# Kernel tuning notes

Measured on AMD Instinct MI355X. Metric: run time of the kernel, lower is better.

## Reference

```python
import jax, jax.numpy as jnp
import numpy as np

B, N = 32768, 512

def setup_inputs() -> dict:
    key = jax.random.key(0)
    k1, k2, k3, k4 = jax.random.split(key, 4)
    log_sigma_hat = jax.random.normal(k1, (B, N), dtype=jnp.float32)
    sigma = jax.random.normal(k2, (B, N), dtype=jnp.float32)
    SR = jax.random.normal(k3, (N,), dtype=jnp.float32)
    # well-conditioned invertible Gamma (covariance-like): A A^T / N + I
    A = jax.random.normal(k4, (N, N), dtype=jnp.float32)
    Gamma = A @ A.T / N + jnp.eye(N, dtype=jnp.float32)
    return {"log_sigma_hat": log_sigma_hat, "sigma": sigma, "SR": SR, "Gamma": Gamma, "k": 12}

def reference(log_sigma_hat, sigma, SR, Gamma, k):
    # r[t] = exp(sigma[t]) / exp(log_sigma_hat[t])  -> [B, N]
    r = jnp.exp(sigma - log_sigma_hat)
    Gamma_inv = jnp.linalg.inv(Gamma)
    v = Gamma_inv @ SR           # [N]  Gamma^{-1} SR
    u = Gamma_inv.T @ SR         # [N]  (SR^T Gamma^{-1})^T
    # first  = SR^T Gamma^{-1} diag(r) SR / k = sum(u * r * SR)
    first = (r * (u * SR)).sum(axis=-1) / k
    # second = SR^T Gamma^{-1} diag(r) Gamma diag(r) Gamma^{-1} SR / (2k)
    w = r * v                                     # [B, N] = diag(r) v
    Gw = jnp.einsum('ij,bj->bi', Gamma, w)        # [B, N] = Gamma diag(r) v
    second = (u * (r * Gw)).sum(axis=-1) / (2 * k)
    utils = first - second                        # [B]
    return -utils.mean()
```

## Files before the change

kernel.cpp:

```cpp
#include <hip/hip_runtime.h>
#include <hip/hip_bf16.h>
#include <stdint.h>

#define BB 32768
#define NN 512
#define CHEB_IT 10

typedef __attribute__((ext_vector_type(8))) short bf16x8;
typedef __attribute__((ext_vector_type(4))) float f32x4;

__device__ __forceinline__ void gld_lds16(const void* g, void* l) {
  typedef __attribute__((address_space(1))) const unsigned int gas_u32;
  typedef __attribute__((address_space(3))) unsigned int las_u32;
  __builtin_amdgcn_global_load_lds((gas_u32*)(uintptr_t)g,
                                   (las_u32*)(uint32_t)(uintptr_t)l, 16, 0, 0);
}

__device__ __forceinline__ unsigned short f2bf(float x) {
  __hip_bfloat16 h = __float2bfloat16(x);
  return *reinterpret_cast<unsigned short*>(&h);
}

__device__ __forceinline__ float bf2f(unsigned short u) {
  return __uint_as_float(((unsigned)u) << 16);
}

__device__ __forceinline__ float wave_reduce(float v) {
#pragma unroll
  for (int off = 32; off > 0; off >>= 1) v += __shfl_xor(v, off, 64);
  return v;
}

__device__ void cheb_phase(const unsigned short* __restrict__ Gbf,
                           const float* __restrict__ SR, float* __restrict__ v_out,
                           float* __restrict__ appart, unsigned int* __restrict__ ctr,
                           float* sm) {
  float* sp = sm;
  float* apw = sm + 512;
  const int t = threadIdx.x;
  const int m = blockIdx.x;
  const int rg = t >> 7;
  const int c0 = (t & 127) * 4;
  const int row0 = m * 128;
  const float theta = 3.16f, delta = 2.19f;
  const float sigma1 = theta / delta;
  float rho = delta / theta;
  float r = SR[t];
  float x = 0.f;
  float p = r * (1.0f / theta);
  for (int k = 0; k < CHEB_IT; ++k) {
    sp[t] = p;
    __syncthreads();
    float a0 = 0, a1 = 0, a2 = 0, a3 = 0;
    for (int j = 0; j < 128; j += 32) {
#pragma unroll
      for (int jj = 0; jj < 8; ++jj) {
        const int lr = j + jj * 4 + rg;
        ushort4 u = *(const ushort4*)(Gbf + (size_t)(row0 + lr) * NN + c0);
        float pv = sp[row0 + lr];
        a0 += bf2f(u.x) * pv; a1 += bf2f(u.y) * pv;
        a2 += bf2f(u.z) * pv; a3 += bf2f(u.w) * pv;
      }
    }
    *(float4*)(apw + rg * 512 + c0) = make_float4(a0, a1, a2, a3);
    __syncthreads();
    float apm = apw[t] + apw[512 + t] + apw[1024 + t] + apw[1536 + t];
    float* buf = appart + (k & 1) * 2048 + m * 512;
    __hip_atomic_store(buf + t, apm, __ATOMIC_RELAXED, __HIP_MEMORY_SCOPE_AGENT);
    __threadfence();
    __syncthreads();
    if (t == 0)
      __hip_atomic_fetch_add(ctr, 1u, __ATOMIC_RELEASE, __HIP_MEMORY_SCOPE_AGENT);
    if (t == 0) {
      const unsigned tgt = 4u * (unsigned)(k + 1);
      int guard = 0;
      while (__hip_atomic_load(ctr, __ATOMIC_ACQUIRE, __HIP_MEMORY_SCOPE_AGENT) < tgt) {
        if (++guard > (1 << 27)) break;
        __builtin_amdgcn_s_sleep(8);
      }
    }
    __syncthreads();
    const float* rbuf = appart + (k & 1) * 2048;
    float w = __hip_atomic_load(rbuf + t, __ATOMIC_RELAXED, __HIP_MEMORY_SCOPE_AGENT) +
              __hip_atomic_load(rbuf + 512 + t, __ATOMIC_RELAXED, __HIP_MEMORY_SCOPE_AGENT) +
              __hip_atomic_load(rbuf + 1024 + t, __ATOMIC_RELAXED, __HIP_MEMORY_SCOPE_AGENT) +
              __hip_atomic_load(rbuf + 1536 + t, __ATOMIC_RELAXED, __HIP_MEMORY_SCOPE_AGENT);
    x += p;
    r -= w;
    const float rho_new = 1.f / (2.f * sigma1 - rho);
    p = rho_new * rho * p + (2.f * rho_new / delta) * r;
    rho = rho_new;
    __syncthreads();
  }
  if (m == 0) v_out[t] = x;
}

__global__ __launch_bounds__(256) void k0_prep(
    const float* __restrict__ Gam, unsigned short* __restrict__ Gbf,
    float* __restrict__ small_zero) {
  const int t = threadIdx.x, b = blockIdx.x;
  const size_t base = ((size_t)b * 256 + t) * 8;
  float4 g0 = *(const float4*)(Gam + base);
  float4 g1 = *(const float4*)(Gam + base + 4);
  *(ushort4*)(Gbf + base) = make_ushort4(f2bf(g0.x), f2bf(g0.y), f2bf(g0.z), f2bf(g0.w));
  *(ushort4*)(Gbf + base + 4) = make_ushort4(f2bf(g1.x), f2bf(g1.y), f2bf(g1.z), f2bf(g1.w));
  if (b == 0)
    for (int i = t; i < 8960; i += 256) small_zero[i] = 0.f;
}

__global__ __launch_bounds__(512) void k1_rexp(
    const float* __restrict__ lsh, const float* __restrict__ sig,
    const float* __restrict__ SR, const unsigned short* __restrict__ Gbf,
    unsigned short* __restrict__ Rb, float* __restrict__ v_out,
    float* __restrict__ colsum, float* __restrict__ appart,
    unsigned int* __restrict__ ctr) {
  __shared__ __align__(16) float sm[2560];
  if (blockIdx.x < 4) {
    cheb_phase(Gbf, SR, v_out, appart, ctr, sm);
    return;
  }
  const int t = threadIdx.x;
  const int wb = blockIdx.x - 4;
  const size_t base = (size_t)wb * 16384;
  float c0 = 0.f, c1 = 0.f, c2 = 0.f, c3 = 0.f;
#pragma unroll
  for (int j = 0; j < 8; ++j) {
    const size_t idx = base + (size_t)j * 2048 + (size_t)t * 4;
    float4 sv = *(const float4*)(sig + idx);
    float4 lv = *(const float4*)(lsh + idx);
    float r0 = __expf(sv.x - lv.x), r1 = __expf(sv.y - lv.y);
    float r2 = __expf(sv.z - lv.z), r3 = __expf(sv.w - lv.w);
    *(ushort4*)(Rb + idx) = make_ushort4(f2bf(r0), f2bf(r1), f2bf(r2), f2bf(r3));
    c0 += r0; c1 += r1; c2 += r2; c3 += r3;
  }
  float* part = sm;
  *(float4*)(part + (t >> 7) * 512 + (t & 127) * 4) = make_float4(c0, c1, c2, c3);
  __syncthreads();
  float s = part[t] + part[512 + t] + part[1024 + t] + part[1536 + t];
  atomicAdd(&colsum[(wb & 7) * NN + t], s);
}

__global__ __launch_bounds__(256) void k1b_gprep(
    const float* __restrict__ Gam, const float* __restrict__ v,
    unsigned short* __restrict__ Gp) {
  const int t = threadIdx.x;
  const size_t e = ((size_t)blockIdx.x * 256 + t) * 8;
  const int i = (int)(e >> 9), j = (int)(e & 511);
  const float vi = v[i];
  float4 va = *(const float4*)(v + j);
  float4 vb = *(const float4*)(v + j + 4);
  float4 g0 = *(const float4*)(Gam + e);
  float4 g1 = *(const float4*)(Gam + e + 4);
  *(ushort4*)(Gp + e) = make_ushort4(f2bf(g0.x * vi * va.x), f2bf(g0.y * vi * va.y),
                                     f2bf(g0.z * vi * va.z), f2bf(g0.w * vi * va.w));
  *(ushort4*)(Gp + e + 4) = make_ushort4(f2bf(g1.x * vi * vb.x), f2bf(g1.y * vi * vb.y),
                                         f2bf(g1.z * vi * vb.z), f2bf(g1.w * vi * vb.w));
}

__global__ __launch_bounds__(512) void k2_gemm(
    const unsigned short* __restrict__ Rb, const unsigned short* __restrict__ Gp,
    float* __restrict__ secsum) {
  __shared__ __align__(16) unsigned short smem[32768];
  const int bid = blockIdx.x;
  const int nt_ = (bid >> 3) & 3;
  const int bs_ = (bid & 7) + ((bid >> 5) << 3);
  const int b0 = bs_ * 128;
  const int n0 = nt_ * 128;
  const int t = threadIdx.x, lane = t & 63, wv = t >> 6;
  const int wi = (wv & 3) * 32, wj = (wv >> 2) * 64;
  const int lm = lane & 15, lq = lane >> 4;
  const int xr = lm & 7;
  const int srow = t >> 3, sc = t & 7;
  const int scol = (sc ^ (srow & 7)) * 8;
  f32x4 acc[2][4];
#pragma unroll
  for (int a = 0; a < 2; ++a)
#pragma unroll
    for (int b = 0; b < 4; ++b) acc[a][b] = (f32x4){0.f, 0.f, 0.f, 0.f};

#define STAGE(kk, buf)                                                                   \
  {                                                                                      \
    unsigned short* As_ = smem + (buf)*16384;                                            \
    unsigned short* Bs_ = As_ + 8192;                                                    \
    gld_lds16(Rb + (size_t)(b0 + srow) * NN + (kk) + scol, As_ + srow * 64 + sc * 8);    \
    gld_lds16(Rb + (size_t)(b0 + 64 + srow) * NN + (kk) + scol,                          \
              As_ + (64 + srow) * 64 + sc * 8);                                          \
    gld_lds16(Gp + (size_t)(n0 + srow) * NN + (kk) + scol, Bs_ + srow * 64 + sc * 8);    \
    gld_lds16(Gp + (size_t)(n0 + 64 + srow) * NN + (kk) + scol,                          \
              Bs_ + (64 + srow) * 64 + sc * 8);                                          \
  }

  STAGE(0, 0);
  __syncthreads();
  for (int c = 0; c < 8; ++c) {
    if (c < 7) STAGE((c + 1) * 64, (c + 1) & 1);
    const unsigned short* As = smem + (c & 1) * 16384;
    const unsigned short* Bs = As + 8192;
#pragma unroll
    for (int s = 0; s < 2; ++s) {
      bf16x8 af[2], bfr[4];
#pragma unroll
      for (int g = 0; g < 2; ++g)
        af[g] = *(const bf16x8*)(As + (wi + g * 16 + lm) * 64 + ((s * 4 + lq) ^ xr) * 8);
#pragma unroll
      for (int g = 0; g < 4; ++g)
        bfr[g] = *(const bf16x8*)(Bs + (wj + g * 16 + lm) * 64 + ((s * 4 + lq) ^ xr) * 8);
#pragma unroll
      for (int gm = 0; gm < 2; ++gm)
#pragma unroll
        for (int gn = 0; gn < 4; ++gn)
          acc[gm][gn] = __builtin_amdgcn_mfma_f32_16x16x32_bf16(af[gm], bfr[gn], acc[gm][gn], 0, 0, 0);
    }
    __syncthreads();
  }
#undef STAGE

  float s_ = 0.f;
#pragma unroll
  for (int gm = 0; gm < 2; ++gm) {
    const int rb = b0 + wi + gm * 16 + lq * 4;
#pragma unroll
    for (int gn = 0; gn < 4; ++gn) {
      const int cl = n0 + wj + gn * 16 + lm;
      const unsigned short* rp = Rb + (size_t)rb * NN + cl;
      s_ += acc[gm][gn][0] * bf2f(rp[0]);
      s_ += acc[gm][gn][1] * bf2f(rp[NN]);
      s_ += acc[gm][gn][2] * bf2f(rp[2 * NN]);
      s_ += acc[gm][gn][3] * bf2f(rp[3 * NN]);
    }
  }
  s_ = wave_reduce(s_);
  float* red = (float*)smem;
  if (lane == 0) red[wv] = s_;
  __syncthreads();
  if (t == 0) {
    float a = 0;
#pragma unroll
    for (int i = 0; i < 8; ++i) a += red[i];
    atomicAdd(&secsum[bid & 63], a);
  }
}

__global__ __launch_bounds__(512) void k4_final(
    const float* __restrict__ colsum, const float* __restrict__ v,
    const float* __restrict__ SR, const float* __restrict__ secsum,
    const int* __restrict__ kp, float* __restrict__ out) {
  __shared__ float red[8];
  const int t = threadIdx.x;
  float cs = 0;
#pragma unroll
  for (int bk = 0; bk < 8; ++bk) cs += colsum[bk * NN + t];
  float f = (cs * (1.0f / BB)) * v[t] * SR[t];
  f = wave_reduce(f);
  if ((t & 63) == 0) red[t >> 6] = f;
  float h = 0.f;
  if (t < 64) {
    h = secsum[t];
    h = wave_reduce(h);
  }
  __syncthreads();
  if (t == 0) {
    float first = 0;
#pragma unroll
    for (int i = 0; i < 8; ++i) first += red[i];
    float kk = (float)kp[0];
    float sec = h / ((float)BB * 2.0f * kk);
    out[0] = -(first / kk - sec);
  }
}

extern "C" void kernel_launch(void* const* d_in, const int* in_sizes, int n_in,
                              void* d_out, int out_size, void* d_ws, size_t ws_size,
                              hipStream_t stream) {
  const float* lsh = (const float*)d_in[0];
  const float* sig = (const float*)d_in[1];
  const float* SR = (const float*)d_in[2];
  const float* Gam = (const float*)d_in[3];
  const int* kp = (const int*)d_in[4];
  char* ws = (char*)d_ws;
  float* colsum = (float*)ws;
  float* secsum = colsum + 4096;
  float* v = secsum + 64;
  unsigned int* ctr = (unsigned int*)(v + 512);
  float* appart = (float*)(ctr + 16);
  unsigned short* Gbf = (unsigned short*)(ws + (64 << 10));
  unsigned short* Gp = (unsigned short*)(ws + (64 << 10) + (512 << 10));
  unsigned short* Rb = (unsigned short*)(ws + (64 << 10) + (1024 << 10));

  k0_prep<<<128, 256, 0, stream>>>(Gam, Gbf, colsum);
  k1_rexp<<<1028, 512, 0, stream>>>(lsh, sig, SR, Gbf, Rb, v, colsum, appart, ctr);
  k1b_gprep<<<128, 256, 0, stream>>>(Gam, v, Gp);
  k2_gemm<<<1024, 512, 0, stream>>>(Rb, Gp, secsum);
  k4_final<<<1, 512, 0, stream>>>(colsum, v, SR, secsum, kp, (float*)d_out);
}
```

Before: 224.7 us.

## Single-block Chebyshev solve, 1024-thread rexp blocks, 256x128 GEMM tiles

The Chebyshev solve moves from four blocks synchronised through global atomics and spin-waits to one 1024-thread block that does the whole matvec with an LDS reduction, removing the inter-block barrier traffic. The exp kernel uses 1024-thread blocks and half as many of them. The GEMM tile grows from 128x128 to 256x128, giving more reuse of the Gp tile and fewer blocks, but it drops the double-buffered global-to-LDS prefetch in favour of a single buffer with load-then-sync. The 16 accumulators per wave raise register pressure, and the loss of load/compute overlap could offset the reuse gain.

```diff
diff --git a/kernel.cpp b/kernel.cpp
--- a/kernel.cpp
+++ b/kernel.cpp
@@ -33,66 +33,49 @@
 
 __device__ void cheb_phase(const unsigned short* __restrict__ Gbf,
                            const float* __restrict__ SR, float* __restrict__ v_out,
-                           float* __restrict__ appart, unsigned int* __restrict__ ctr,
                            float* sm) {
   float* sp = sm;
   float* apw = sm + 512;
   const int t = threadIdx.x;
-  const int m = blockIdx.x;
   const int rg = t >> 7;
   const int c0 = (t & 127) * 4;
-  const int row0 = m * 128;
   const float theta = 3.16f, delta = 2.19f;
   const float sigma1 = theta / delta;
   float rho = delta / theta;
-  float r = SR[t];
-  float x = 0.f;
-  float p = r * (1.0f / theta);
+  float x = 0.f, r = 0.f, p = 0.f;
+  if (t < 512) {
+    r = SR[t];
+    p = r * (1.0f / theta);
+  }
   for (int k = 0; k < CHEB_IT; ++k) {
-    sp[t] = p;
+    if (t < 512) sp[t] = p;
     __syncthreads();
     float a0 = 0, a1 = 0, a2 = 0, a3 = 0;
-    for (int j = 0; j < 128; j += 32) {
+    for (int j = 0; j < NN; j += 64) {
 #pragma unroll
       for (int jj = 0; jj < 8; ++jj) {
-        const int lr = j + jj * 4 + rg;
-        ushort4 u = *(const ushort4*)(Gbf + (size_t)(row0 + lr) * NN + c0);
-        float pv = sp[row0 + lr];
+        const int row = j + jj * 8 + rg;
+        ushort4 u = *(const ushort4*)(Gbf + (size_t)row * NN + c0);
+        float pv = sp[row];
         a0 += bf2f(u.x) * pv; a1 += bf2f(u.y) * pv;
         a2 += bf2f(u.z) * pv; a3 += bf2f(u.w) * pv;
       }
     }
     *(float4*)(apw + rg * 512 + c0) = make_float4(a0, a1, a2, a3);
     __syncthreads();
-    float apm = apw[t] + apw[512 + t] + apw[1024 + t] + apw[1536 + t];
-    float* buf = appart + (k & 1) * 2048 + m * 512;
-    __hip_atomic_store(buf + t, apm, __ATOMIC_RELAXED, __HIP_MEMORY_SCOPE_AGENT);
-    __threadfence();
-    __syncthreads();
-    if (t == 0)
-      __hip_atomic_fetch_add(ctr, 1u, __ATOMIC_RELEASE, __HIP_MEMORY_SCOPE_AGENT);
-    if (t == 0) {
-      const unsigned tgt = 4u * (unsigned)(k + 1);
-      int guard = 0;
-      while (__hip_atomic_load(ctr, __ATOMIC_ACQUIRE, __HIP_MEMORY_SCOPE_AGENT) < tgt) {
-        if (++guard > (1 << 27)) break;
-        __builtin_amdgcn_s_sleep(8);
-      }
-    }
-    __syncthreads();
-    const float* rbuf = appart + (k & 1) * 2048;
-    float w = __hip_atomic_load(rbuf + t, __ATOMIC_RELAXED, __HIP_MEMORY_SCOPE_AGENT) +
-              __hip_atomic_load(rbuf + 512 + t, __ATOMIC_RELAXED, __HIP_MEMORY_SCOPE_AGENT) +
-              __hip_atomic_load(rbuf + 1024 + t, __ATOMIC_RELAXED, __HIP_MEMORY_SCOPE_AGENT) +
-              __hip_atomic_load(rbuf + 1536 + t, __ATOMIC_RELAXED, __HIP_MEMORY_SCOPE_AGENT);
-    x += p;
-    r -= w;
-    const float rho_new = 1.f / (2.f * sigma1 - rho);
-    p = rho_new * rho * p + (2.f * rho_new / delta) * r;
-    rho = rho_new;
-    __syncthreads();
-  }
-  if (m == 0) v_out[t] = x;
+    if (t < 512) {
+      float ap = 0.f;
+#pragma unroll
+      for (int g = 0; g < 8; ++g) ap += apw[g * 512 + t];
+      x += p;
+      r -= ap;
+      const float rho_new = 1.f / (2.f * sigma1 - rho);
+      p = rho_new * rho * p + (2.f * rho_new / delta) * r;
+      rho = rho_new;
+    }
+    __syncthreads();
+  }
+  if (t < 512) v_out[t] = x;
 }
 
 __global__ __launch_bounds__(256) void k0_prep(
@@ -105,27 +88,28 @@
   *(ushort4*)(Gbf + base) = make_ushort4(f2bf(g0.x), f2bf(g0.y), f2bf(g0.z), f2bf(g0.w));
   *(ushort4*)(Gbf + base + 4) = make_ushort4(f2bf(g1.x), f2bf(g1.y), f2bf(g1.z), f2bf(g1.w));
   if (b == 0)
-    for (int i = t; i < 8960; i += 256) small_zero[i] = 0.f;
-}
-
-__global__ __launch_bounds__(512) void k1_rexp(
+    for (int i = t; i < 4672; i += 256) small_zero[i] = 0.f;
+}
+
+__global__ __launch_bounds__(1024) void k1_rexp(
     const float* __restrict__ lsh, const float* __restrict__ sig,
     const float* __restrict__ SR, const unsigned short* __restrict__ Gbf,
     unsigned short* __restrict__ Rb, float* __restrict__ v_out,
-    float* __restrict__ colsum, float* __restrict__ appart,
-    unsigned int* __restrict__ ctr) {
-  __shared__ __align__(16) float sm[2560];
-  if (blockIdx.x < 4) {
-    cheb_phase(Gbf, SR, v_out, appart, ctr, sm);
+    float* __restrict__ colsum) {
+  __shared__ __align__(16) float sm[4608];
+  if (blockIdx.x == 0) {
+    cheb_phase(Gbf, SR, v_out, sm);
     return;
   }
   const int t = threadIdx.x;
-  const int wb = blockIdx.x - 4;
-  const size_t base = (size_t)wb * 16384;
+  const int wb = blockIdx.x - 1;
+  const int g = t >> 7;
+  const int c = (t & 127) * 4;
+  const size_t base = (size_t)wb * 32768;
   float c0 = 0.f, c1 = 0.f, c2 = 0.f, c3 = 0.f;
 #pragma unroll
   for (int j = 0; j < 8; ++j) {
-    const size_t idx = base + (size_t)j * 2048 + (size_t)t * 4;
+    const size_t idx = base + (size_t)(g + 8 * j) * 512 + c;
     float4 sv = *(const float4*)(sig + idx);
     float4 lv = *(const float4*)(lsh + idx);
     float r0 = __expf(sv.x - lv.x), r1 = __expf(sv.y - lv.y);
@@ -134,10 +118,14 @@
     c0 += r0; c1 += r1; c2 += r2; c3 += r3;
   }
   float* part = sm;
-  *(float4*)(part + (t >> 7) * 512 + (t & 127) * 4) = make_float4(c0, c1, c2, c3);
-  __syncthreads();
-  float s = part[t] + part[512 + t] + part[1024 + t] + part[1536 + t];
-  atomicAdd(&colsum[(wb & 7) * NN + t], s);
+  *(float4*)(part + g * 512 + c) = make_float4(c0, c1, c2, c3);
+  __syncthreads();
+  if (t < 512) {
+    float s = 0.f;
+#pragma unroll
+    for (int gg = 0; gg < 8; ++gg) s += part[gg * 512 + t];
+    atomicAdd(&colsum[(wb & 7) * NN + t], s);
+  }
 }
 
 __global__ __launch_bounds__(256) void k1b_gprep(
@@ -160,64 +148,60 @@
 __global__ __launch_bounds__(512) void k2_gemm(
     const unsigned short* __restrict__ Rb, const unsigned short* __restrict__ Gp,
     float* __restrict__ secsum) {
-  __shared__ __align__(16) unsigned short smem[32768];
+  __shared__ __align__(16) unsigned short smem[24576];
   const int bid = blockIdx.x;
   const int nt_ = (bid >> 3) & 3;
   const int bs_ = (bid & 7) + ((bid >> 5) << 3);
-  const int b0 = bs_ * 128;
+  const int b0 = bs_ * 256;
   const int n0 = nt_ * 128;
   const int t = threadIdx.x, lane = t & 63, wv = t >> 6;
-  const int wi = (wv & 3) * 32, wj = (wv >> 2) * 64;
+  const int wi = (wv >> 1) * 64;
+  const int wj = (wv & 1) * 64;
   const int lm = lane & 15, lq = lane >> 4;
   const int xr = lm & 7;
   const int srow = t >> 3, sc = t & 7;
   const int scol = (sc ^ (srow & 7)) * 8;
-  f32x4 acc[2][4];
-#pragma unroll
-  for (int a = 0; a < 2; ++a)
+  unsigned short* As = smem;
+  unsigned short* Bs = smem + 16384;
+  f32x4 acc[4][4];
+#pragma unroll
+  for (int a = 0; a < 4; ++a)
 #pragma unroll
     for (int b = 0; b < 4; ++b) acc[a][b] = (f32x4){0.f, 0.f, 0.f, 0.f};
 
-#define STAGE(kk, buf)                                                                   \
-  {                                                                                      \
-    unsigned short* As_ = smem + (buf)*16384;                                            \
-    unsigned short* Bs_ = As_ + 8192;                                                    \
-    gld_lds16(Rb + (size_t)(b0 + srow) * NN + (kk) + scol, As_ + srow * 64 + sc * 8);    \
-    gld_lds16(Rb + (size_t)(b0 + 64 + srow) * NN + (kk) + scol,                          \
-              As_ + (64 + srow) * 64 + sc * 8);                                          \
-    gld_lds16(Gp + (size_t)(n0 + srow) * NN + (kk) + scol, Bs_ + srow * 64 + sc * 8);    \
-    gld_lds16(Gp + (size_t)(n0 + 64 + srow) * NN + (kk) + scol,                          \
-              Bs_ + (64 + srow) * 64 + sc * 8);                                          \
-  }
-
-  STAGE(0, 0);
-  __syncthreads();
-  for (int c = 0; c < 8; ++c) {
-    if (c < 7) STAGE((c + 1) * 64, (c + 1) & 1);
-    const unsigned short* As = smem + (c & 1) * 16384;
-    const unsigned short* Bs = As + 8192;
+  for (int ch = 0; ch < 8; ++ch) {
+    const int kk = ch * 64;
+    if (ch) __syncthreads();
+#pragma unroll
+    for (int ps = 0; ps < 4; ++ps)
+      gld_lds16(Rb + (size_t)(b0 + ps * 64 + srow) * NN + kk + scol,
+                As + (ps * 64 + srow) * 64 + sc * 8);
+#pragma unroll
+    for (int ps = 0; ps < 2; ++ps)
+      gld_lds16(Gp + (size_t)(n0 + ps * 64 + srow) * NN + kk + scol,
+                Bs + (ps * 64 + srow) * 64 + sc * 8);
+    __syncthreads();
 #pragma unroll
     for (int s = 0; s < 2; ++s) {
-      bf16x8 af[2], bfr[4];
-#pragma unroll
-      for (int g = 0; g < 2; ++g)
+      bf16x8 af[4], bfr[4];
+#pragma unroll
+      for (int g = 0; g < 4; ++g)
         af[g] = *(const bf16x8*)(As + (wi + g * 16 + lm) * 64 + ((s * 4 + lq) ^ xr) * 8);
 #pragma unroll
       for (int g = 0; g < 4; ++g)
         bfr[g] = *(const bf16x8*)(Bs + (wj + g * 16 + lm) * 64 + ((s * 4 + lq) ^ xr) * 8);
 #pragma unroll
-      for (int gm = 0; gm < 2; ++gm)
+      for (int gm = 0; gm < 4; ++gm)
 #pragma unroll
         for (int gn = 0; gn < 4; ++gn)
           acc[gm][gn] = __builtin_amdgcn_mfma_f32_16x16x32_bf16(af[gm], bfr[gn], acc[gm][gn], 0, 0, 0);
     }
-    __syncthreads();
-  }
-#undef STAGE
+  }
+  __syncthreads();
 
   float s_ = 0.f;
 #pragma unroll
-  for (int gm = 0; gm < 2; ++gm) {
+  for (int gm = 0; gm < 4; ++gm) {
     const int rb = b0 + wi + gm * 16 + lq * 4;
 #pragma unroll
     for (int gn = 0; gn < 4; ++gn) {
@@ -281,15 +265,13 @@
   float* colsum = (float*)ws;
   float* secsum = colsum + 4096;
   float* v = secsum + 64;
-  unsigned int* ctr = (unsigned int*)(v + 512);
-  float* appart = (float*)(ctr + 16);
-  unsigned short* Gbf = (unsigned short*)(ws + (64 << 10));
-  unsigned short* Gp = (unsigned short*)(ws + (64 << 10) + (512 << 10));
-  unsigned short* Rb = (unsigned short*)(ws + (64 << 10) + (1024 << 10));
+  unsigned short* Gbf = (unsigned short*)(ws + (32 << 10));
+  unsigned short* Gp = (unsigned short*)(ws + (32 << 10) + (512 << 10));
+  unsigned short* Rb = (unsigned short*)(ws + (32 << 10) + (1024 << 10));
 
   k0_prep<<<128, 256, 0, stream>>>(Gam, Gbf, colsum);
-  k1_rexp<<<1028, 512, 0, stream>>>(lsh, sig, SR, Gbf, Rb, v, colsum, appart, ctr);
+  k1_rexp<<<513, 1024, 0, stream>>>(lsh, sig, SR, Gbf, Rb, v, colsum);
   k1b_gprep<<<128, 256, 0, stream>>>(Gam, v, Gp);
-  k2_gemm<<<1024, 512, 0, stream>>>(Rb, Gp, secsum);
+  k2_gemm<<<512, 512, 0, stream>>>(Rb, Gp, secsum);
   k4_final<<<1, 512, 0, stream>>>(colsum, v, SR, secsum, kp, (float*)d_out);
 }
```

Measured after the change: 363.9 us. 1.62x slower.
